# Performance work log

Hardware: AMD Instinct MI355X
Metric: run time of the kernel (lower is better)

The kernel has to match this reference:

```python
import jax, jax.numpy as jnp
import numpy as np

C, K, N = 128, 27, 4096   # channels, kernel offsets (3^3), parent points
M = 8 * N                  # child points (FCG: up to 8 children per parent)


def sp_conv(f, nbr, W):
    # sparse submanifold conv: gather K neighbors then per-offset GEMM
    # f: [P, C], nbr: [P, K], W: [K, C, C] -> [P, C]
    return jnp.einsum('pkc,kcd->pd', f[nbr], W)


def resnet(f, nbr, Wa, Wb):
    h = jax.nn.relu(sp_conv(f, nbr, Wa))
    return jax.nn.relu(sp_conv(h, nbr, Wb) + f)


def setup_inputs():
    key = jax.random.key(0)
    ks = jax.random.split(key, 30)
    conv = lambda k: jax.random.normal(k, (K, C, C), dtype=jnp.float32) * 0.02
    return {
        'x_O': jax.random.randint(ks[0], (N,), 0, 256, dtype=jnp.int32),
        'gt_O': jax.random.randint(ks[1], (M, 1), 0, 256, dtype=jnp.int32),
        'nbr_par': jax.random.randint(ks[2], (N, K), 0, N, dtype=jnp.int32),
        'nbr_child': jax.random.randint(ks[3], (M, K), 0, M, dtype=jnp.int32),
        'child_oct': jnp.tile(jnp.arange(8, dtype=jnp.int32), N),
        'prior_emb': jax.random.normal(ks[4], (256, C), dtype=jnp.float32),
        'pW0': conv(ks[5]), 'pW1a': conv(ks[6]), 'pW1b': conv(ks[7]),
        'pW2a': conv(ks[8]), 'pW2b': conv(ks[9]),
        'oct_emb': jax.random.normal(ks[10], (8, C), dtype=jnp.float32) * 0.1,
        'tW0': conv(ks[11]), 'tW1a': conv(ks[12]), 'tW1b': conv(ks[13]),
        'tW2a': conv(ks[14]), 'tW2b': conv(ks[15]),
        's1_emb': jax.random.normal(ks[16], (16, C), dtype=jnp.float32) * 0.1,
        'h0W1': jax.random.normal(ks[17], (C, C), dtype=jnp.float32) * 0.09,
        'h0b1': jnp.zeros((C,), dtype=jnp.float32),
        'h0W2': jax.random.normal(ks[18], (C, 16), dtype=jnp.float32) * 0.09,
        'h0b2': jnp.zeros((16,), dtype=jnp.float32),
        'h1W1': jax.random.normal(ks[19], (C, C), dtype=jnp.float32) * 0.09,
        'h1b1': jnp.zeros((C,), dtype=jnp.float32),
        'h1W2': jax.random.normal(ks[20], (C, 16), dtype=jnp.float32) * 0.09,
        'h1b2': jnp.zeros((16,), dtype=jnp.float32),
    }


def reference(x_O, gt_O, nbr_par, nbr_child, child_oct,
              prior_emb, pW0, pW1a, pW1b, pW2a, pW2b,
              oct_emb, tW0, tW1a, tW1b, tW2a, tW2b, s1_emb,
              h0W1, h0b1, h0W2, h0b2, h1W1, h1b1, h1W2, h1b2):
    # prior branch: occupancy byte embedding + sparse ResNet stack
    f = prior_emb[x_O]                                   # [N, C]
    f = jax.nn.relu(sp_conv(f, nbr_par, pW0))
    f = resnet(f, nbr_par, pW1a, pW1b)
    f = resnet(f, nbr_par, pW2a, pW2b)
    # FCG: broadcast parent feature to its 8 children; TargetEmbedding adds octant embedding
    g = jnp.repeat(f, 8, axis=0) + oct_emb[child_oct]    # [M, C]
    g = jax.nn.relu(sp_conv(g, nbr_child, tW0))
    g = resnet(g, nbr_child, tW1a, tW1b)
    g = resnet(g, nbr_child, tW2a, tW2b)
    # two-stage 4-bit occupancy prediction + gather-based entropy
    gt_s0 = jnp.remainder(gt_O, 16)                      # [M, 1]
    gt_s1 = gt_O // 16
    p0 = jax.nn.softmax(jax.nn.relu(g @ h0W1 + h0b1) @ h0W2 + h0b2, axis=-1)
    g1 = g + s1_emb[gt_s0[:, 0]]
    p1 = jax.nn.softmax(jax.nn.relu(g1 @ h1W1 + h1b1) @ h1W2 + h1b2, axis=-1)
    b0 = jnp.take_along_axis(p0, gt_s0, axis=1)
    b1 = jnp.take_along_axis(p1, gt_s1, axis=1)
    bits = (jnp.sum(jnp.clip(-jnp.log2(b0 + 1e-10), 0.0, 50.0))
            + jnp.sum(jnp.clip(-jnp.log2(b1 + 1e-10), 0.0, 50.0)))
    return bits / jnp.float32(N)
```

## Files before the change

### kernel.cpp

```cpp
#include <hip/hip_runtime.h>

typedef unsigned int u32;
typedef unsigned short u16;
typedef unsigned char u8;
typedef short bf16x8 __attribute__((ext_vector_type(8)));
typedef float f32x4 __attribute__((ext_vector_type(4)));
typedef unsigned short u16x4 __attribute__((ext_vector_type(4)));
typedef long lx2 __attribute__((ext_vector_type(2)));

#define KOFF 27

__device__ __forceinline__ float bf2f(u16 u) {
    u32 x = ((u32)u) << 16;
    return __builtin_bit_cast(float, x);
}
__device__ __forceinline__ u16 f2bf(float f) {
    u32 u = __builtin_bit_cast(u32, f);
    u32 r = (u + 0x7FFFu + ((u >> 16) & 1u)) >> 16;
    return (u16)r;
}
__device__ __forceinline__ u8 f2fp8(float f) {
    u32 u = __builtin_bit_cast(u32, f);
    u32 sign = (u >> 24) & 0x80u;
    float a = fabsf(f);
    if (a >= 448.f) return (u8)(sign | 0x7Eu);
    if (a < 0.015625f) {
        int q = (int)rintf(a * 512.f);
        return (u8)(sign | (u32)q);
    }
    u32 m = u & 0x7FFFFFFFu;
    m += 0x7FFFFu + ((m >> 20) & 1u);
    u32 e8 = (m >> 23) - 120u;
    if (e8 >= 16u) return (u8)(sign | 0x7Eu);
    return (u8)(sign | (e8 << 3) | ((m >> 20) & 7u));
}
__device__ __forceinline__ float fp82f(u8 v) {
    u32 s = ((u32)(v & 0x80)) << 24;
    u32 em = v & 0x7Fu;
    float mag;
    if (em < 8)
        mag = (float)em * 0.001953125f;
    else
        mag = __builtin_bit_cast(float,
                                 (((em >> 3) + 120u) << 23) | ((em & 7u) << 20));
    return __builtin_bit_cast(float, __builtin_bit_cast(u32, mag) | s);
}
__device__ __forceinline__ void async16(void* lds, const void* g) {
    __builtin_amdgcn_global_load_lds(
        (const __attribute__((address_space(1))) u32*)g,
        (__attribute__((address_space(3))) u32*)lds, 16, 0, 0);
}

struct PrepArgs {
    const float* ws[12];
    u16* wd[12];
    u8* wd3[5];
    const float* h0W2;
    const float* h1W2;
    u16* wt2h;
    const float* s1emb;
    const float* h1W1f;
    float* E1;
};
__global__ __launch_bounds__(256) void prep_mega(PrepArgs a) {
    __shared__ float t[128][65];
    const int bid = blockIdx.x;
    if (bid < 270) {
        const int w = bid / 54, r = bid % 54;
        const int k = r >> 1, cg = r & 1;
        const float* s = a.ws[w] + k * 16384 + cg * 64;
        for (int i = threadIdx.x; i < 8192; i += 256) {
            int c = i >> 6, dl = i & 63;
            t[c][dl] = s[c * 128 + dl];
        }
        __syncthreads();
        u16* ob = a.wd[w] + k * 16384;
        for (int sl = threadIdx.x; sl < 1024; sl += 256) {
            int lane = sl & 63, kk2 = (sl >> 6) & 1, n = (sl >> 7) & 3,
                kslc = (sl >> 9) & 1;
            int S = (((kslc * 2 + cg) * 4 + n) * 2 + kk2) * 64 + lane;
            int dl = n * 16 + (lane & 15);
            int c0 = kslc * 64 + kk2 * 32 + (lane >> 4) * 8;
            u16x4 v0, v1;
#pragma unroll
            for (int j = 0; j < 4; ++j) v0[j] = f2bf(t[c0 + j][dl]);
#pragma unroll
            for (int j = 0; j < 4; ++j) v1[j] = f2bf(t[c0 + 4 + j][dl]);
            *(u16x4*)(ob + S * 8) = v0;
            *(u16x4*)(ob + S * 8 + 4) = v1;
        }
    } else if (bid < 540) {
        const int idx = bid - 270;
        const int w5 = idx / 54, r = idx % 54;
        const int k = r >> 1, cg = r & 1;
        const float* s = a.ws[5 + w5] + k * 16384 + cg * 64;
        for (int i = threadIdx.x; i < 8192; i += 256) {
            int c = i >> 6, dl = i & 63;
            t[c][dl] = s[c * 128 + dl];
        }
        __syncthreads();
        u8* ob = a.wd3[w5] + k * 16384;
        for (int sl = threadIdx.x; sl < 8192; sl += 256) {
            int j = sl & 7, lane = (sl >> 3) & 63, kk2 = (sl >> 9) & 1,
                n = (sl >> 10) & 3, kslc = (sl >> 12) & 1;
            int c = kslc * 64 + kk2 * 32 + (lane >> 4) * 8 + j;
            int dl = n * 16 + (lane & 15);
            int byte = (kslc * 2 + cg) * 4096 + n * 1024 + lane * 16 + kk2 * 8 + j;
            ob[byte] = f2fp8(t[c][dl]);
        }
    } else if (bid < 544) {
        int r = bid - 540;
        int w = 10 + (r >> 1), half = r & 1;
        const float* s = a.ws[w] + half * 64;
        for (int i = threadIdx.x; i < 8192; i += 256) {
            int c = i >> 6, dl = i & 63;
            t[c][dl] = s[c * 128 + dl];
        }
        __syncthreads();
        u16* db = a.wd[w];
        for (int i = threadIdx.x; i < 8192; i += 256) {
            int dl = i >> 7, c = i & 127;
            int d = half * 64 + dl;
            db[d * 128 + (c ^ ((d & 7) << 3))] = f2bf(t[c][dl]);
        }
    } else if (bid < 546) {
        int h = bid - 544;
        const float* src = h ? a.h1W2 : a.h0W2;
        u16* dst = a.wt2h + h * 2048;
        for (int i = threadIdx.x; i < 2048; i += 256) {
            int j = i >> 7, d = i & 127;
            dst[j * 128 + (d ^ ((j & 7) << 3))] = f2bf(src[d * 16 + j]);
        }
    } else {
        int b = bid - 546;
        int r = b * 2 + (threadIdx.x >> 7);
        int c = threadIdx.x & 127;
        float acc = 0.f;
        for (int kx = 0; kx < 128; ++kx)
            acc = fmaf(a.s1emb[r * 128 + kx], a.h1W1f[kx * 128 + c], acc);
        a.E1[r * 128 + c] = acc;
    }
}

__global__ __launch_bounds__(256) void embed_k(const int* __restrict__ xO,
                                               const float* __restrict__ emb,
                                               u16* __restrict__ out) {
    int idx = blockIdx.x * 256 + threadIdx.x;
    int c = idx & 127, n = idx >> 7;
    out[idx] = f2bf(emb[xO[n] * 128 + c]);
}

__global__ __launch_bounds__(256) void expand8(const u16* __restrict__ f,
                                               const int* __restrict__ oct,
                                               const float* __restrict__ oemb,
                                               u8* __restrict__ g) {
    int idx = blockIdx.x * 256 + threadIdx.x;
    int c = idx & 127, m = idx >> 7;
    g[idx] = f2fp8(bf2f(f[(m >> 3) * 128 + c]) + oemb[oct[m] * 128 + c]);
}

#define LOADB(dst, vb, imm)                                      \
    asm volatile("global_load_dwordx4 %0, %1, %2 offset:" #imm   \
                 : "=&v"(dst)                                    \
                 : "v"(vb), "s"(wk)                              \
                 : "memory")

template <bool PARTIAL>
__global__ __launch_bounds__(256, 2) void conv7(
    const u16* __restrict__ fin, const int* __restrict__ nbr,
    const u16* __restrict__ wt, const u16* __restrict__ res,
    u16* __restrict__ fout, float* __restrict__ pout, int npts) {
    constexpr int BM = 64;
    __shared__ __align__(16) u16 Asb[2][4][4096];
    __shared__ int nbrS[BM * KOFF];
    const int tid = threadIdx.x;
    const int wid = tid >> 6;
    const int lane = tid & 63;
    const int p0 = blockIdx.x * BM;
    const int g = PARTIAL ? blockIdx.y : 0;
    const int k0 = PARTIAL ? (g * KOFF) >> 3 : 0;
    const int k1 = PARTIAL ? ((g + 1) * KOFF) >> 3 : KOFF;

    for (int i = tid; i < BM * KOFF; i += 256)
        nbrS[i] = nbr[(p0 + i / KOFF) * KOFF + (i % KOFF)];
    __syncthreads();

    f32x4 acc[2][4];
#pragma unroll
    for (int m = 0; m < 2; ++m)
#pragma unroll
        for (int n = 0; n < 4; ++n) acc[m][n] = f32x4{0.f, 0.f, 0.f, 0.f};

    const int rg0 = (wid >> 1) * 32;
    const int cg = wid & 1;
    const int lrow = lane & 15;
    const int lkb = (lane >> 4) * 16;
    const int b0a = cg * 8192 + lane * 16;
    const int b0b = b0a + 4096;
    const int b1a = b0a + 16384;
    const int b1b = b1a + 4096;

    auto stageA = [&](int k, int buf) {
        char* db = (char*)&Asb[buf][wid][0];
#pragma unroll
        for (int i = 0; i < 8; ++i) {
            int rl = i * 4 + (lane >> 4);
            int cbs = ((lane & 15) * 16) ^ ((rl & 7) << 4);
            int rgl = nbrS[(rg0 + rl) * KOFF + k];
            async16(db + i * 1024, (const char*)fin + (size_t)rgl * 256 + cbs);
        }
    };
    auto loadB = [&](int k, bf16x8 (&B)[16]) {
        const u16* wk = wt + k * 16384;
        LOADB(B[0], b0a, 0);
        LOADB(B[1], b0a, 1024);
        LOADB(B[2], b1a, 0);
        LOADB(B[3], b1a, 1024);
        LOADB(B[4], b0a, 2048);
        LOADB(B[5], b0a, 3072);
        LOADB(B[6], b1a, 2048);
        LOADB(B[7], b1a, 3072);
        LOADB(B[8], b0b, 0);
        LOADB(B[9], b0b, 1024);
        LOADB(B[10], b1b, 0);
        LOADB(B[11], b1b, 1024);
        LOADB(B[12], b0b, 2048);
        LOADB(B[13], b0b, 3072);
        LOADB(B[14], b1b, 2048);
        LOADB(B[15], b1b, 3072);
    };

    bf16x8 Ba[16], Bb[16];
    stageA(k0, 0);
    loadB(k0, Ba);

    auto body = [&](bf16x8 (&Bc)[16], bf16x8 (&Bn)[16], int k) {
        const int ab = (k - k0) & 1;
        if (k + 1 < k1) {
            stageA(k + 1, ab ^ 1);
            loadB(k + 1, Bn);
            asm volatile("s_waitcnt vmcnt(24)" ::: "memory");
        } else {
            asm volatile("s_waitcnt vmcnt(0)" ::: "memory");
        }
        __builtin_amdgcn_sched_barrier(0);
        const char* AsW = (const char*)&Asb[ab][wid][0];
        __builtin_amdgcn_s_setprio(1);
#pragma unroll
        for (int kk = 0; kk < 4; ++kk) {
            bf16x8 av[2];
#pragma unroll
            for (int m = 0; m < 2; ++m) {
                int row = m * 16 + lrow;
                int cb = (kk * 64 + lkb) ^ ((row & 7) << 4);
                av[m] = *(const bf16x8*)(AsW + row * 256 + cb);
            }
#pragma unroll
            for (int m = 0; m < 2; ++m)
#pragma unroll
                for (int n = 0; n < 4; ++n)
                    acc[m][n] = __builtin_amdgcn_mfma_f32_16x16x32_bf16(
                        av[m], Bc[n * 4 + kk], acc[m][n], 0, 0, 0);
        }
        __builtin_amdgcn_s_setprio(0);
    };

    int k = k0;
    while (true) {
        body(Ba, Bb, k);
        if (++k >= k1) break;
        body(Bb, Ba, k);
        if (++k >= k1) break;
    }

    if constexpr (PARTIAL) {
        float* pg = pout + (size_t)g * npts * 128;
#pragma unroll
        for (int m = 0; m < 2; ++m) {
            int prow = p0 + rg0 + m * 16 + (lane >> 4) * 4;
#pragma unroll
            for (int n = 0; n < 4; ++n) {
                int dcol = cg * 64 + n * 16 + lrow;
#pragma unroll
                for (int q = 0; q < 4; ++q)
                    pg[(prow + q) * 128 + dcol] = acc[m][n][q];
            }
        }
    } else {
#pragma unroll
        for (int m = 0; m < 2; ++m) {
            int prow = p0 + rg0 + m * 16 + (lane >> 4) * 4;
#pragma unroll
            for (int n = 0; n < 4; ++n) {
                int dcol = cg * 64 + n * 16 + lrow;
#pragma unroll
                for (int q = 0; q < 4; ++q) {
                    float v = acc[m][n][q];
                    int p = prow + q;
                    if (res) v += bf2f(res[p * 128 + dcol]);
                    v = v > 0.f ? v : 0.f;
                    fout[p * 128 + dcol] = f2bf(v);
                }
            }
        }
    }
}

template <bool LASTBF16>
__global__ __launch_bounds__(256, 4) void conv9(
    const u8* __restrict__ fin, const int* __restrict__ nbr,
    const u8* __restrict__ wt, const u8* __restrict__ res,
    void* __restrict__ fout_) {
    constexpr int BM = 32;
    __shared__ __align__(16) u8 Asb[3][BM * 128];
    __shared__ float red[4096];
    __shared__ int nbrS[BM * KOFF];
    const int tid = threadIdx.x;
    const int wid = tid >> 6;
    const int lane = tid & 63;
    const int p0 = blockIdx.x * BM;

    for (int i = tid; i < BM * KOFF; i += 256)
        nbrS[i] = nbr[(p0 + i / KOFF) * KOFF + (i % KOFF)];
    __syncthreads();

    f32x4 acc[2][4];
#pragma unroll
    for (int m = 0; m < 2; ++m)
#pragma unroll
        for (int n = 0; n < 4; ++n) acc[m][n] = f32x4{0.f, 0.f, 0.f, 0.f};

    const int kslc = wid >> 1;
    const int CB = (wid & 1) * 64;
    const int lrow = lane & 15;
    const int vb = (kslc * 2 + (wid & 1)) * 4096 + lane * 16;

    auto stageA = [&](int k, int buf) {
        int rl = wid * 8 + (lane >> 3);
        int boff = (lane & 7) * 16;
        int rg = nbrS[rl * KOFF + k];
        async16((char*)&Asb[buf][0] + wid * 1024,
                (const char*)fin + (size_t)rg * 128 + (boff ^ ((rl & 7) << 4)));
    };
    auto loadB = [&](int k, lx2 (&B)[4]) {
        const u8* wk = wt + k * 16384;
        LOADB(B[0], vb, 0);
        LOADB(B[1], vb, 1024);
        LOADB(B[2], vb, 2048);
        LOADB(B[3], vb, 3072);
    };

    lx2 Ba4[4], Bb4[4];
    loadB(0, Ba4);
    stageA(0, 0);
    stageA(1, 1);

    auto body = [&](lx2 (&Bc)[4], lx2 (&Bn)[4], int k) {
        __builtin_amdgcn_s_barrier();
        const int kB = (k + 1 < KOFF) ? k + 1 : KOFF - 1;
        const int kA = (k + 2 < KOFF) ? k + 2 : KOFF - 1;
        loadB(kB, Bn);
        stageA(kA, (k + 2) % 3);
        asm volatile("s_waitcnt vmcnt(6)" ::: "memory");
        __builtin_amdgcn_s_barrier();
        __builtin_amdgcn_sched_barrier(0);
        __builtin_amdgcn_s_setprio(1);
        const u8* As = &Asb[k % 3][0];
#pragma unroll
        for (int kk2 = 0; kk2 < 2; ++kk2) {
            long av[2];
#pragma unroll
            for (int m = 0; m < 2; ++m) {
                int row = m * 16 + lrow;
                int off = (kslc * 64 + kk2 * 32 + (lane >> 4) * 8) ^
                          ((row & 7) << 4);
                av[m] = *(const long*)((const char*)As + row * 128 + off);
            }
#pragma unroll
            for (int m = 0; m < 2; ++m)
#pragma unroll
                for (int n = 0; n < 4; ++n)
                    acc[m][n] = __builtin_amdgcn_mfma_f32_16x16x32_fp8_fp8(
                        av[m], Bc[n][kk2], acc[m][n], 0, 0, 0);
        }
        __builtin_amdgcn_s_setprio(0);
    };

    int k = 0;
    while (true) {
        body(Ba4, Bb4, k);
        if (++k >= KOFF) break;
        body(Bb4, Ba4, k);
        if (++k >= KOFF) break;
    }

    __syncthreads();
    if (kslc == 1) {
        const int base = (wid - 2) * 2048;
#pragma unroll
        for (int m = 0; m < 2; ++m)
#pragma unroll
            for (int n = 0; n < 4; ++n)
#pragma unroll
                for (int q = 0; q < 4; ++q)
                    red[base + (((m * 4 + n) * 4 + q) * 64) + lane] =
                        acc[m][n][q];
    }
    __syncthreads();
    if (kslc == 0) {
        const int base = wid * 2048;
#pragma unroll
        for (int m = 0; m < 2; ++m)
#pragma unroll
            for (int n = 0; n < 4; ++n)
#pragma unroll
                for (int q = 0; q < 4; ++q)
                    acc[m][n][q] +=
                        red[base + (((m * 4 + n) * 4 + q) * 64) + lane];
#pragma unroll
        for (int m = 0; m < 2; ++m) {
            int prow = p0 + m * 16 + (lane >> 4) * 4;
#pragma unroll
            for (int n = 0; n < 4; ++n) {
                int dcol = CB + n * 16 + lrow;
#pragma unroll
                for (int q = 0; q < 4; ++q) {
                    float v = acc[m][n][q];
                    int p = prow + q;
                    if (res) v += fp82f(res[p * 128 + dcol]);
                    v = v > 0.f ? v : 0.f;
                    if constexpr (LASTBF16)
                        ((u16*)fout_)[p * 128 + dcol] = f2bf(v);
                    else
                        ((u8*)fout_)[p * 128 + dcol] = f2fp8(v);
                }
            }
        }
    }
}

__global__ __launch_bounds__(256) void combine_k(const float* __restrict__ P,
                                                 const u16* __restrict__ res,
                                                 u16* __restrict__ fout,
                                                 int nelem) {
    int base = (blockIdx.x * 256 + threadIdx.x) * 4;
    f32x4 s = *(const f32x4*)(P + base);
#pragma unroll
    for (int gg = 1; gg < 8; ++gg)
        s += *(const f32x4*)(P + (size_t)gg * nelem + base);
    u16x4 o;
    if (res) {
        u16x4 rv = *(const u16x4*)(res + base);
#pragma unroll
        for (int j = 0; j < 4; ++j) s[j] += bf2f(rv[j]);
    }
#pragma unroll
    for (int j = 0; j < 4; ++j) {
        float v = s[j] > 0.f ? s[j] : 0.f;
        o[j] = f2bf(v);
    }
    *(u16x4*)(fout + base) = o;
}

__global__ __launch_bounds__(512, 1) void fused_heads(
    const u16* __restrict__ G, const int* __restrict__ gtO,
    const u16* __restrict__ wt2, const u16* __restrict__ wt2h,
    const float* __restrict__ b1a, const float* __restrict__ b1b,
    const float* __restrict__ E1, const float* __restrict__ b2a,
    const float* __restrict__ b2b, float* __restrict__ partial) {
    __shared__ __align__(16) u16 AB[49152];
    __shared__ __align__(16) u16 W2ts[4096];
    __shared__ float E1s[2048];
    __shared__ float b2s[32];
    __shared__ int gts[256];
    __shared__ float bitsS[256];
    u16* Asb = AB;
    u16* Bsb = AB + 16384;
    char* Hb = (char*)AB;
    const int tid = threadIdx.x, wid = tid >> 6, lane = tid & 63;
    const int lrow = lane & 15, lkb = (lane >> 4) * 16;
    const int p0 = blockIdx.x * 128;

#pragma unroll
    for (int i = 0; i < 4; ++i) {
        int o = i * 8192 + tid * 16;
        int r = o >> 8;
        int cbs = (o & 255) ^ ((r & 7) << 4);
        async16((char*)Asb + i * 8192 + wid * 1024,
                (const char*)G + (size_t)(p0 + r) * 256 + cbs);
    }
#pragma unroll
    for (int i = 0; i < 8; ++i)
        async16((char*)Bsb + i * 8192 + wid * 1024,
                (const char*)wt2 + i * 8192 + tid * 16);
    async16((char*)W2ts + wid * 1024, (const char*)wt2h + tid * 16);
    for (int i = tid; i < 2048; i += 512) E1s[i] = E1[i];
    if (tid < 16) b2s[tid] = b2a[tid];
    else if (tid < 32) b2s[tid] = b2b[tid - 16];
    if (tid < 128) {
        int g = gtO[p0 + tid];
        gts[tid] = g & 15;
        gts[128 + tid] = g >> 4;
    }
    __syncthreads();

    const int RB = (wid >> 1) * 32, CB = (wid & 1) * 128;
    f32x4 acc[2][8];
#pragma unroll
    for (int m = 0; m < 2; ++m)
#pragma unroll
        for (int n = 0; n < 8; ++n) acc[m][n] = f32x4{0.f, 0.f, 0.f, 0.f};
    __builtin_amdgcn_s_setprio(1);
#pragma unroll
    for (int kk = 0; kk < 4; ++kk) {
        bf16x8 av[2], bv[8];
#pragma unroll
        for (int m = 0; m < 2; ++m) {
            int row = RB + m * 16 + lrow;
            int cb = (kk * 64 + lkb) ^ ((row & 7) << 4);
            av[m] = *(const bf16x8*)((const char*)Asb + row * 256 + cb);
        }
#pragma unroll
        for (int n = 0; n < 8; ++n) {
            int drow = CB + n * 16 + lrow;
            int cb = (kk * 64 + lkb) ^ ((drow & 7) << 4);
            bv[n] = *(const bf16x8*)((const char*)Bsb + drow * 256 + cb);
        }
#pragma unroll
        for (int m = 0; m < 2; ++m)
#pragma unroll
            for (int n = 0; n < 8; ++n)
                acc[m][n] = __builtin_amdgcn_mfma_f32_16x16x32_bf16(
                    av[m], bv[n], acc[m][n], 0, 0, 0);
    }
    __builtin_amdgcn_s_setprio(0);
    __syncthreads();

    const float* b1p = CB ? b1b : b1a;
    float b1v[8];
#pragma unroll
    for (int n = 0; n < 8; ++n) b1v[n] = b1p[n * 16 + lrow];
#pragma unroll
    for (int m = 0; m < 2; ++m) {
#pragma unroll
        for (int q = 0; q < 4; ++q) {
            int p = RB + m * 16 + (lane >> 4) * 4 + q;
#pragma unroll
            for (int n = 0; n < 8; ++n) {
                float v = acc[m][n][q] + b1v[n];
                if (CB) v += E1s[gts[p] * 128 + n * 16 + lrow];
                v = v > 0.f ? v : 0.f;
                int colb = (CB + n * 16 + lrow) * 2;
                *(u16*)(Hb + p * 512 + (colb ^ ((p & 7) << 4))) = f2bf(v);
            }
        }
    }
    __syncthreads();

    const int RB2 = wid * 16;
    f32x4 acc2[2];
    acc2[0] = f32x4{0.f, 0.f, 0.f, 0.f};
    acc2[1] = f32x4{0.f, 0.f, 0.f, 0.f};
#pragma unroll
    for (int kk = 0; kk < 4; ++kk) {
        int row = RB2 + lrow;
        int cb = (kk * 64 + lkb) ^ ((row & 7) << 4);
        int cbw = (kk * 64 + lkb) ^ ((lrow & 7) << 4);
#pragma unroll
        for (int h = 0; h < 2; ++h) {
            bf16x8 a2 = *(const bf16x8*)(Hb + row * 512 + h * 256 + cb);
            bf16x8 b2v = *(const bf16x8*)((const char*)W2ts + h * 4096 +
                                          lrow * 256 + cbw);
            acc2[h] = __builtin_amdgcn_mfma_f32_16x16x32_bf16(a2, b2v, acc2[h],
                                                              0, 0, 0);
        }
    }
    const int jj = lrow;
#pragma unroll
    for (int h = 0; h < 2; ++h) {
#pragma unroll
        for (int q = 0; q < 4; ++q) {
            int pt = RB2 + (lane >> 4) * 4 + q;
            float v = acc2[h][q] + b2s[h * 16 + jj];
            float mx = v;
#pragma unroll
            for (int o = 1; o < 16; o <<= 1) mx = fmaxf(mx, __shfl_xor(mx, o, 16));
            float e = expf(v - mx);
            float s = e;
#pragma unroll
            for (int o = 1; o < 16; o <<= 1) s += __shfl_xor(s, o, 16);
            float bits = -log2f(e / s + 1e-10f);
            bits = fminf(fmaxf(bits, 0.f), 50.f);
            if (jj == gts[h * 128 + pt]) bitsS[h * 128 + pt] = bits;
        }
    }
    __syncthreads();
    if (tid < 64) {
        float s = bitsS[tid] + bitsS[tid + 64] + bitsS[tid + 128] + bitsS[tid + 192];
#pragma unroll
        for (int o = 32; o > 0; o >>= 1) s += __shfl_down(s, o, 64);
        if (tid == 0) partial[blockIdx.x] = s;
    }
}

__global__ __launch_bounds__(256) void finalize_k(const float* __restrict__ partial,
                                                  float* __restrict__ out, int n) {
    float s = 0.f;
    for (int i = threadIdx.x; i < n; i += 256) s += partial[i];
#pragma unroll
    for (int o = 32; o > 0; o >>= 1) s += __shfl_down(s, o, 64);
    __shared__ float wsum[4];
    if ((threadIdx.x & 63) == 0) wsum[threadIdx.x >> 6] = s;
    __syncthreads();
    if (threadIdx.x == 0)
        out[0] = (wsum[0] + wsum[1] + wsum[2] + wsum[3]) * (1.0f / 4096.0f);
}

extern "C" void kernel_launch(void* const* d_in, const int* in_sizes, int n_in,
                              void* d_out, int out_size, void* d_ws,
                              size_t ws_size, hipStream_t stream) {
    const int N = 4096, M = 32768;
    const int* x_O = (const int*)d_in[0];
    const int* gt_O = (const int*)d_in[1];
    const int* nbr_par = (const int*)d_in[2];
    const int* nbr_ch = (const int*)d_in[3];
    const int* child_oct = (const int*)d_in[4];
    const float* prior_emb = (const float*)d_in[5];
    const float* convW[10] = {
        (const float*)d_in[6],  (const float*)d_in[7],  (const float*)d_in[8],
        (const float*)d_in[9],  (const float*)d_in[10], (const float*)d_in[12],
        (const float*)d_in[13], (const float*)d_in[14], (const float*)d_in[15],
        (const float*)d_in[16]};
    const float* oct_emb = (const float*)d_in[11];
    const float* s1_emb = (const float*)d_in[17];
    const float* h0W1 = (const float*)d_in[18];
    const float* h0b1 = (const float*)d_in[19];
    const float* h0W2 = (const float*)d_in[20];
    const float* h0b2 = (const float*)d_in[21];
    const float* h1W1 = (const float*)d_in[22];
    const float* h1b1 = (const float*)d_in[23];
    const float* h1W2 = (const float*)d_in[24];
    const float* h1b2 = (const float*)d_in[25];

    char* ws = (char*)d_ws;
    size_t off = 0;
    auto alloc = [&](size_t b) {
        void* p = ws + off;
        off += (b + 255) & ~(size_t)255;
        return p;
    };
    PrepArgs pa;
    for (int i = 0; i < 10; ++i) pa.ws[i] = convW[i];
    for (int i = 0; i < 5; ++i) pa.wd[i] = (u16*)alloc(27 * 128 * 128 * 2);
    for (int i = 5; i < 10; ++i) pa.wd[i] = nullptr;
    for (int i = 0; i < 5; ++i) pa.wd3[i] = (u8*)alloc(27 * 128 * 128);
    u16* Wt2 = (u16*)alloc(256 * 128 * 2);
    pa.ws[10] = h0W1;
    pa.ws[11] = h1W1;
    pa.wd[10] = Wt2;
    pa.wd[11] = Wt2 + 128 * 128;
    u16* wt2h = (u16*)alloc(2 * 16 * 128 * 2);
    float* E1 = (float*)alloc(16 * 128 * 4);
    pa.h0W2 = h0W2;
    pa.h1W2 = h1W2;
    pa.wt2h = wt2h;
    pa.s1emb = s1_emb;
    pa.h1W1f = h1W1;
    pa.E1 = E1;

    u16* fA = (u16*)alloc((size_t)N * 256);
    u16* fB = (u16*)alloc((size_t)N * 256);
    u16* fC = (u16*)alloc((size_t)N * 256);
    u8* g8A = (u8*)alloc((size_t)M * 128);
    u8* g8B = (u8*)alloc((size_t)M * 128);
    u8* g8C = (u8*)alloc((size_t)M * 128);
    u16* gBF = (u16*)alloc((size_t)M * 256);
    float* partial = (float*)alloc(256 * 4);
    float* pconv = (float*)g8A;

    prep_mega<<<554, 256, 0, stream>>>(pa);
    embed_k<<<N * 128 / 256, 256, 0, stream>>>(x_O, prior_emb, fA);

    const int PE = N * 128;
    conv7<true><<<dim3(64, 8), 256, 0, stream>>>(fA, nbr_par, pa.wd[0], nullptr, nullptr, pconv, N);
    combine_k<<<PE / 1024, 256, 0, stream>>>(pconv, nullptr, fB, PE);
    conv7<true><<<dim3(64, 8), 256, 0, stream>>>(fB, nbr_par, pa.wd[1], nullptr, nullptr, pconv, N);
    combine_k<<<PE / 1024, 256, 0, stream>>>(pconv, nullptr, fC, PE);
    conv7<true><<<dim3(64, 8), 256, 0, stream>>>(fC, nbr_par, pa.wd[2], nullptr, nullptr, pconv, N);
    combine_k<<<PE / 1024, 256, 0, stream>>>(pconv, fB, fA, PE);
    conv7<true><<<dim3(64, 8), 256, 0, stream>>>(fA, nbr_par, pa.wd[3], nullptr, nullptr, pconv, N);
    combine_k<<<PE / 1024, 256, 0, stream>>>(pconv, nullptr, fC, PE);
    conv7<true><<<dim3(64, 8), 256, 0, stream>>>(fC, nbr_par, pa.wd[4], nullptr, nullptr, pconv, N);
    combine_k<<<PE / 1024, 256, 0, stream>>>(pconv, fA, fB, PE);

    expand8<<<M * 128 / 256, 256, 0, stream>>>(fB, child_oct, oct_emb, g8A);

    conv9<false><<<1024, 256, 0, stream>>>(g8A, nbr_ch, pa.wd3[0], nullptr, g8B);
    conv9<false><<<1024, 256, 0, stream>>>(g8B, nbr_ch, pa.wd3[1], nullptr, g8C);
    conv9<false><<<1024, 256, 0, stream>>>(g8C, nbr_ch, pa.wd3[2], g8B, g8A);
    conv9<false><<<1024, 256, 0, stream>>>(g8A, nbr_ch, pa.wd3[3], nullptr, g8C);
    conv9<true><<<1024, 256, 0, stream>>>(g8C, nbr_ch, pa.wd3[4], g8A, gBF);

    fused_heads<<<M / 128, 512, 0, stream>>>(gBF, gt_O, Wt2, wt2h, h0b1, h1b1,
                                             E1, h0b2, h1b2, partial);
    finalize_k<<<1, 256, 0, stream>>>(partial, (float*)d_out, 256);

    (void)in_sizes; (void)n_in; (void)out_size; (void)ws_size;
}
```

Baseline: 304.7 us.

## Process two kernel offsets per barrier phase in child sparse conv

```diff
diff --git a/kernel.cpp b/kernel.cpp
--- a/kernel.cpp
+++ b/kernel.cpp
@@ -307,12 +307,12 @@
 }
 
 template <bool LASTBF16>
-__global__ __launch_bounds__(256, 4) void conv9(
+__global__ __launch_bounds__(256, 4) void conv10(
     const u8* __restrict__ fin, const int* __restrict__ nbr,
     const u8* __restrict__ wt, const u8* __restrict__ res,
     void* __restrict__ fout_) {
     constexpr int BM = 32;
-    __shared__ __align__(16) u8 Asb[3][BM * 128];
+    __shared__ __align__(16) u8 Asb[2][2][BM * 128];
     __shared__ float red[4096];
     __shared__ int nbrS[BM * KOFF];
     const int tid = threadIdx.x;
@@ -335,11 +335,11 @@
     const int lrow = lane & 15;
     const int vb = (kslc * 2 + (wid & 1)) * 4096 + lane * 16;
 
-    auto stageA = [&](int k, int buf) {
+    auto stageA = [&](int k, int buf, int slot) {
         int rl = wid * 8 + (lane >> 3);
         int boff = (lane & 7) * 16;
         int rg = nbrS[rl * KOFF + k];
-        async16((char*)&Asb[buf][0] + wid * 1024,
+        async16((char*)&Asb[buf][slot][0] + wid * 1024,
                 (const char*)fin + (size_t)rg * 128 + (boff ^ ((rl & 7) << 4)));
     };
     auto loadB = [&](int k, lx2 (&B)[4]) {
@@ -349,23 +349,7 @@
         LOADB(B[2], vb, 2048);
         LOADB(B[3], vb, 3072);
     };
-
-    lx2 Ba4[4], Bb4[4];
-    loadB(0, Ba4);
-    stageA(0, 0);
-    stageA(1, 1);
-
-    auto body = [&](lx2 (&Bc)[4], lx2 (&Bn)[4], int k) {
-        __builtin_amdgcn_s_barrier();
-        const int kB = (k + 1 < KOFF) ? k + 1 : KOFF - 1;
-        const int kA = (k + 2 < KOFF) ? k + 2 : KOFF - 1;
-        loadB(kB, Bn);
-        stageA(kA, (k + 2) % 3);
-        asm volatile("s_waitcnt vmcnt(6)" ::: "memory");
-        __builtin_amdgcn_s_barrier();
-        __builtin_amdgcn_sched_barrier(0);
-        __builtin_amdgcn_s_setprio(1);
-        const u8* As = &Asb[k % 3][0];
+    auto mmaSlot = [&](const u8* As, lx2 (&B)[4]) {
 #pragma unroll
         for (int kk2 = 0; kk2 < 2; ++kk2) {
             long av[2];
@@ -381,17 +365,33 @@
 #pragma unroll
                 for (int n = 0; n < 4; ++n)
                     acc[m][n] = __builtin_amdgcn_mfma_f32_16x16x32_fp8_fp8(
-                        av[m], Bc[n][kk2], acc[m][n], 0, 0, 0);
-        }
+                        av[m], B[n][kk2], acc[m][n], 0, 0, 0);
+        }
+    };
+
+    lx2 Bs0[4], Bs1[4];
+    stageA(0, 0, 0);
+    stageA(1, 0, 1);
+
+    constexpr int NPH = (KOFF + 1) / 2;
+#pragma unroll 1
+    for (int ph = 0; ph < NPH; ++ph) {
+        const int buf = ph & 1;
+        __builtin_amdgcn_s_barrier();
+        const int kb1 = (2 * ph + 1 < KOFF) ? 2 * ph + 1 : KOFF - 1;
+        loadB(2 * ph, Bs0);
+        loadB(kb1, Bs1);
+        const int kn0 = (2 * ph + 2 < KOFF) ? 2 * ph + 2 : KOFF - 1;
+        const int kn1 = (2 * ph + 3 < KOFF) ? 2 * ph + 3 : KOFF - 1;
+        stageA(kn0, buf ^ 1, 0);
+        stageA(kn1, buf ^ 1, 1);
+        asm volatile("s_waitcnt vmcnt(2)" ::: "memory");
+        __builtin_amdgcn_s_barrier();
+        __builtin_amdgcn_sched_barrier(0);
+        __builtin_amdgcn_s_setprio(1);
+        mmaSlot(&Asb[buf][0][0], Bs0);
+        if (2 * ph + 1 < KOFF) mmaSlot(&Asb[buf][1][0], Bs1);
         __builtin_amdgcn_s_setprio(0);
-    };
-
-    int k = 0;
-    while (true) {
-        body(Ba4, Bb4, k);
-        if (++k >= KOFF) break;
-        body(Bb4, Ba4, k);
-        if (++k >= KOFF) break;
     }
 
     __syncthreads();
@@ -695,11 +695,11 @@
 
     expand8<<<M * 128 / 256, 256, 0, stream>>>(fB, child_oct, oct_emb, g8A);
 
-    conv9<false><<<1024, 256, 0, stream>>>(g8A, nbr_ch, pa.wd3[0], nullptr, g8B);
-    conv9<false><<<1024, 256, 0, stream>>>(g8B, nbr_ch, pa.wd3[1], nullptr, g8C);
-    conv9<false><<<1024, 256, 0, stream>>>(g8C, nbr_ch, pa.wd3[2], g8B, g8A);
-    conv9<false><<<1024, 256, 0, stream>>>(g8A, nbr_ch, pa.wd3[3], nullptr, g8C);
-    conv9<true><<<1024, 256, 0, stream>>>(g8C, nbr_ch, pa.wd3[4], g8A, gBF);
+    conv10<false><<<1024, 256, 0, stream>>>(g8A, nbr_ch, pa.wd3[0], nullptr, g8B);
+    conv10<false><<<1024, 256, 0, stream>>>(g8B, nbr_ch, pa.wd3[1], nullptr, g8C);
+    conv10<false><<<1024, 256, 0, stream>>>(g8C, nbr_ch, pa.wd3[2], g8B, g8A);
+    conv10<false><<<1024, 256, 0, stream>>>(g8A, nbr_ch, pa.wd3[3], nullptr, g8C);
+    conv10<true><<<1024, 256, 0, stream>>>(g8C, nbr_ch, pa.wd3[4], g8A, gBF);
 
     fused_heads<<<M / 128, 512, 0, stream>>>(gBF, gt_O, Wt2, wt2h, h0b1, h1b1,
                                              E1, h0b2, h1b2, partial);
```

Measured after the change: 302.4 us. No clear change (-0.7%).
